# Optimization experiments

Measured on AMD Instinct MI355X. Metric: run time of the kernel, lower is better.

The kernel has to match this reference:

```python
import jax, jax.numpy as jnp
import numpy as np

N = 10000            # nodes
E = 320000           # edges (avg degree 32)
L = 4                # layers
S = 64               # hidden 0e multiplicity
V = 16               # hidden 1o multiplicity
EMB = 32             # node-attr embedding dim
NB = 8               # bessel basis per channel (r and v -> 2*NB edge feats)
MR = 2.5             # max_radius
DEG = 32.0           # num_neighbors
GS = S + V           # gate input scalars: 64 scalars + 16 gates
NW = S * 2 + V * 2 + V * 2   # 192 per-edge tensor-product weights
MAXT = 100           # max atom types


def _semi_unitary(K):
    # Newton-Schulz orthogonalization: K^T K -> I (semi-unitary uplift matrix)
    K = K / jnp.linalg.norm(K)
    for _ in range(10):
        K = 1.5 * K - 0.5 * K @ (K.T @ K)
    return K


def _smooth_cutoff(t):
    u = 2.0 * (t - 1.0)
    y = (1.0 - jnp.cos(jnp.pi * u)) * 0.5
    return jnp.where(u > 0, 0.0, jnp.where(u < -1.0, 1.0, y))


def _edge_geom(d):
    # d: (E,3) edge vector. Returns cutoff-weighted 1x1o SH (component norm) and bessel features.
    r = jnp.linalg.norm(d, axis=1)                       # (E,)
    sh = np.sqrt(3.0) * d / r[:, None]                   # spherical harmonics 1x1o
    attr = _smooth_cutoff(r / MR)[:, None] * sh          # (E,3)
    k = jnp.arange(1, NB + 1, dtype=jnp.float32) * jnp.pi
    feat = np.sqrt(2.0 / MR) * jnp.sin(k * (r / MR)[:, None]) / r[:, None]
    return attr, feat * np.sqrt(NB)                      # (E,3), (E,NB)


def _fctp(s, v, attr, Ws, Wv):
    # FullyConnectedTensorProduct with pure-scalar (0e) node attr == attr-weighted per-irrep linear
    os = jnp.einsum('ni,ne,oie->no', s, attr, Ws) / np.sqrt(s.shape[1] * EMB)
    ov = jnp.einsum('nim,ne,oie->nom', v, attr, Wv) / np.sqrt(v.shape[1] * EMB)
    return os, ov


def _forward(x, node_attr, edge_src, edge_dst, emb_table, PU_K, h, mix,
             si_Ws, si_Wv, sc_Ws, sc_Wv, lin1_Ws, lin1_Wv, lin2_Ws, lin2_Wv,
             fc_W1, fc_b1, fc_W2, fc_b2, fc_W3, fc_b3):
    attr = emb_table[node_attr]                          # (N,EMB)
    K = _semi_unitary(PU_K)                              # (V,2)
    yv = jnp.einsum('ui,nim->num', K, x.reshape(N, 2, 3))  # uplift vectors
    ys = jnp.zeros((N, S), x.dtype)
    ys_old, yv_old = ys, yv
    c_s, c_x = np.sin(np.pi / 8), np.cos(np.pi / 8)
    for i in range(L):
        ar, fr = _edge_geom(x[:, :3][edge_src] - x[:, :3][edge_dst])
        av, fv = _edge_geom(x[:, 3:][edge_src] - x[:, 3:][edge_dst])
        a = jnp.stack([ar, av], axis=1)                  # (E,2,3) = 2x1o edge attr
        ef = jnp.concatenate([fr, fv], axis=1)           # (E,2*NB)
        # radial MLP -> per-edge TP weights
        hd = jax.nn.silu(ef @ fc_W1[i] + fc_b1[i])
        hd = jax.nn.silu(hd @ fc_W2[i] + fc_b2[i])
        w = hd @ fc_W3[i] + fc_b3[i]                     # (E,NW)
        w1 = w[:, :S * 2].reshape(-1, S, 2)
        w2 = w[:, S * 2:S * 2 + V * 2].reshape(-1, V, 2)
        w3 = w[:, S * 2 + V * 2:].reshape(-1, V, 2)
        # conv: lin1 -> gather -> TP -> scatter -> lin2 ; plus self-connection
        fs, fvv = _fctp(ys, yv, attr, lin1_Ws[i], lin1_Wv[i])
        s_src, v_src = fs[edge_src], fvv[edge_src]
        # 0e x 1o -> 1o (uvu)
        o1 = jnp.einsum('euv,eu,evm->eum', w1, s_src, a) / np.sqrt(2.0)   # (E,S,3)
        # 1o x 1o -> 0e (uvu)
        dots = jnp.einsum('eum,evm->euv', v_src, a)
        o2 = jnp.einsum('euv,euv->eu', w2, dots) / np.sqrt(6.0)           # (E,V)
        # 1o x 1o -> 1o (cross, uvu)
        cr = jnp.cross(v_src[:, :, None, :], a[:, None, :, :])            # (E,V,2,3)
        o3 = jnp.einsum('euv,euvm->eum', w3, cr) / 2.0                    # (E,V,3)
        mid_s = jax.ops.segment_sum(o2, edge_dst, num_segments=N) / np.sqrt(DEG)
        mid_v = jax.ops.segment_sum(jnp.concatenate([o1, o3], axis=1), edge_dst,
                                    num_segments=N) / np.sqrt(DEG)        # (N,S+V,3)
        cs2, cv2 = _fctp(mid_s, mid_v, attr, lin2_Ws[i], lin2_Wv[i])      # (N,GS),(N,V,3)
        scs, scv = _fctp(ys, yv, attr, sc_Ws[i], sc_Wv[i])
        conv_s = c_s * scs + c_x * cs2
        conv_v = c_s * scv + c_x * cv2
        # gate: silu scalars, sigmoid gates * gated vectors
        gns = jax.nn.silu(conv_s[:, :S])
        gnv = jax.nn.sigmoid(conv_s[:, S:])[:, :, None] * conv_v
        # self-interaction: per-irrep linear
        sis = ys @ si_Ws[i].T / np.sqrt(S)
        siv = jnp.einsum('oi,nim->nom', si_Wv[i], yv) / np.sqrt(V)
        # leapfrog update
        h2 = h[i] ** 2
        ns = 2.0 * ys - ys_old + h2 * (mix[i] * gns + (mix[i] - 1.0) * sis)
        nv = 2.0 * yv - yv_old + h2 * (mix[i] * gnv + (mix[i] - 1.0) * siv)
        ys_old, yv_old = ys, yv
        ys, yv = ns, nv
        x = jnp.einsum('ui,num->nim', K, yv).reshape(N, 6)   # project
    return x


def setup_inputs() -> dict:
    key = jax.random.key(0)
    ks = jax.random.split(key, 24)
    def g(i, sh, fan=1.0):
        return jax.random.normal(ks[i], sh, dtype=jnp.float32) / np.sqrt(fan)
    edge_src = jax.random.randint(ks[20], (E,), 0, N, dtype=jnp.int32)
    off = jax.random.randint(ks[21], (E,), 1, N, dtype=jnp.int32)
    edge_dst = (edge_src + off) % N                      # guarantees src != dst
    return {
        'x': g(0, (N, 6)),
        'batch': jnp.zeros((N,), jnp.int32),
        'node_attr': jax.random.randint(ks[22], (N,), 0, MAXT, dtype=jnp.int32),
        'edge_src': edge_src,
        'edge_dst': edge_dst,
        'emb_table': g(1, (MAXT, EMB)),
        'PU_K': g(2, (V, 2)),
        'h': jnp.full((L,), 0.01, jnp.float32),
        'mix': jnp.full((L,), 0.5, jnp.float32),
        'si_Ws': g(3, (L, S, S)), 'si_Wv': g(4, (L, V, V)),
        'sc_Ws': g(5, (L, GS, S, EMB)), 'sc_Wv': g(6, (L, V, V, EMB)),
        'lin1_Ws': g(7, (L, S, S, EMB)), 'lin1_Wv': g(8, (L, V, V, EMB)),
        'lin2_Ws': g(9, (L, GS, V, EMB)), 'lin2_Wv': g(10, (L, V, S + V, EMB)),
        'fc_W1': g(11, (L, 2 * NB, 64), 2 * NB), 'fc_b1': jnp.zeros((L, 64), jnp.float32),
        'fc_W2': g(12, (L, 64, 64), 64), 'fc_b2': jnp.zeros((L, 64), jnp.float32),
        'fc_W3': g(13, (L, 64, NW), 64), 'fc_b3': jnp.zeros((L, NW), jnp.float32),
    }


def reference(x, batch, node_attr, edge_src, edge_dst, emb_table, PU_K, h, mix,
              si_Ws, si_Wv, sc_Ws, sc_Wv, lin1_Ws, lin1_Wv, lin2_Ws, lin2_Wv,
              fc_W1, fc_b1, fc_W2, fc_b2, fc_W3, fc_b3):
    return _forward(x, node_attr, edge_src, edge_dst, emb_table, PU_K, h, mix,
                    si_Ws, si_Wv, sc_Ws, sc_Wv, lin1_Ws, lin1_Wv, lin2_Ws, lin2_Wv,
                    fc_W1, fc_b1, fc_W2, fc_b2, fc_W3, fc_b3)
```

## Files before the change

### kernel.cpp

```cpp
#include <hip/hip_runtime.h>
#include <hip/hip_fp8.h>
#include <math.h>

#define NN 10000
#define NE 320000
#define PI_F 3.14159265358979323846f

typedef __attribute__((ext_vector_type(8))) short short8x;
typedef __attribute__((ext_vector_type(4))) float float4x;
typedef __attribute__((ext_vector_type(4))) unsigned short ushort4x;

#if defined(__has_builtin)
#if __has_builtin(__builtin_amdgcn_cvt_pk_fp8_f32) && __has_builtin(__builtin_amdgcn_cvt_f32_fp8)
#define HW_FP8 1
#endif
#endif

__device__ __forceinline__ unsigned short f2b(float f) {
    unsigned b = __float_as_uint(f);
    return (unsigned short)((b + 0x7FFFu + ((b >> 16) & 1u)) >> 16);
}
__device__ __forceinline__ float b2f(unsigned short u) {
    return __uint_as_float(((unsigned)u) << 16);
}
__device__ __forceinline__ float silu(float x) {
    return x / (1.f + __expf(-x));
}
__device__ __forceinline__ unsigned char f2e4(float f) {
#ifdef HW_FP8
    int r = __builtin_amdgcn_cvt_pk_fp8_f32(f, f, 0, false);
    return (unsigned char)(r & 0xff);
#else
    __hip_fp8_e4m3 q(f);
    return (unsigned char)q.__x;
#endif
}
__device__ __forceinline__ float e42f(unsigned char v) {
#ifdef HW_FP8
    return __builtin_amdgcn_cvt_f32_fp8((int)v, 0);
#else
    __hip_fp8_e4m3 q;
    q.__x = (__hip_fp8_storage_t)v;
    return (float)q;
#endif
}
__device__ __forceinline__ float e4sel(unsigned word, int sel) {
#ifdef HW_FP8
    switch (sel & 3) {
        case 0:  return __builtin_amdgcn_cvt_f32_fp8((int)word, 0);
        case 1:  return __builtin_amdgcn_cvt_f32_fp8((int)word, 1);
        case 2:  return __builtin_amdgcn_cvt_f32_fp8((int)word, 2);
        default: return __builtin_amdgcn_cvt_f32_fp8((int)word, 3);
    }
#else
    return e42f((unsigned char)((word >> (8*(sel & 3))) & 0xffu));
#endif
}
__device__ __forceinline__ unsigned pk4(float a, float b, float c, float d) {
#ifdef HW_FP8
    unsigned w = (unsigned)__builtin_amdgcn_cvt_pk_fp8_f32(a, b, 0, false);
    w = (unsigned)__builtin_amdgcn_cvt_pk_fp8_f32(c, d, (int)w, true);
    return w;
#else
    return (unsigned)f2e4(a) | ((unsigned)f2e4(b) << 8) |
           ((unsigned)f2e4(c) << 16) | ((unsigned)f2e4(d) << 24);
#endif
}

__global__ void k_newton_kernel(const float* __restrict__ PU, float* __restrict__ Kout)
{
    if (threadIdx.x != 0 || blockIdx.x != 0) return;
    float K[32];
    float nrm = 0.f;
    for (int i = 0; i < 32; ++i) { K[i] = PU[i]; nrm += K[i]*K[i]; }
    float inv = 1.0f / sqrtf(nrm);
    for (int i = 0; i < 32; ++i) K[i] *= inv;
    for (int it = 0; it < 10; ++it) {
        float m00 = 0.f, m01 = 0.f, m11 = 0.f;
        for (int u = 0; u < 16; ++u) {
            float a = K[2*u], b = K[2*u+1];
            m00 += a*a; m01 += a*b; m11 += b*b;
        }
        for (int u = 0; u < 16; ++u) {
            float a = K[2*u], b = K[2*u+1];
            K[2*u]   = 1.5f*a - 0.5f*(a*m00 + b*m01);
            K[2*u+1] = 1.5f*b - 0.5f*(a*m01 + b*m11);
        }
    }
    for (int i = 0; i < 32; ++i) Kout[i] = K[i];
}

__global__ __launch_bounds__(256) void init_all_kernel(
    const float* __restrict__ x, const float* __restrict__ K,
    float* __restrict__ xp, float* __restrict__ yv0, float* __restrict__ yv1,
    float* __restrict__ ys0, float* __restrict__ ys1, float* __restrict__ fsb)
{
    int tid = blockIdx.x*256 + threadIdx.x;
    if (tid < NN*8) {
        int n = tid >> 3, c = tid & 7;
        xp[tid] = (c < 6) ? x[n*6 + c] : 0.f;
        return;
    }
    int t2 = tid - NN*8;
    if (t2 < NN*48) {
        int n = t2/48, j = t2%48, u = j/3, m = j%3;
        float v = K[2*u]*x[n*6+m] + K[2*u+1]*x[n*6+3+m];
        yv0[t2] = v; yv1[t2] = v;
        return;
    }
    t2 -= NN*48;
    if (t2 < NN*64) { ys0[t2] = 0.f; ys1[t2] = 0.f; fsb[t2] = 0.f; }
}

__global__ void init_fvv_kernel(const float* __restrict__ yv, const int* __restrict__ types,
                                const float* __restrict__ lin1vT0, float* __restrict__ fvv)
{
    int tid = blockIdx.x*blockDim.x + threadIdx.x;
    if (tid >= NN*48) return;
    int n = tid/48, j = tid%48, o = j/3, m = j%3;
    int t = types[n];
    const float* W = lin1vT0 + (size_t)t*256;
    float acc = 0.f;
    #pragma unroll
    for (int i = 0; i < 16; ++i) acc += yv[n*48 + i*3 + m]*W[i*16 + o];
    fvv[tid] = acc;
}

__device__ __forceinline__ void be_body(const float* __restrict__ W, const float* __restrict__ emb,
                                        float* __restrict__ out, int id, int O, int I, float scale)
{
    int o = id % O; int r = id / O;
    int i = r % I; r /= I;
    int t = r % 100; int l = r / 100;
    const float* w  = W + (((size_t)l*O + o)*I + i)*32;
    const float* em = emb + (size_t)t*32;
    float acc = 0.f;
    #pragma unroll
    for (int e = 0; e < 32; ++e) acc += w[e]*em[e];
    out[id] = acc*scale;
}

#define PREP_TOTAL (2048000 + 1638400 + 512000 + 512000 + 102400 + 102400 + 49152 + 16384 + 16384 + 8192 + 1024)
__global__ __launch_bounds__(256) void prep_kernel(
    const float* __restrict__ lin1_Ws, const float* __restrict__ lin1_Wv,
    const float* __restrict__ sc_Ws,   const float* __restrict__ sc_Wv,
    const float* __restrict__ lin2_Ws, const float* __restrict__ lin2_Wv,
    const float* __restrict__ si_Ws,   const float* __restrict__ si_Wv,
    const float* __restrict__ fc_W1,   const float* __restrict__ fc_W2,
    const float* __restrict__ fc_W3,   const float* __restrict__ emb,
    float* __restrict__ lin1sT, float* __restrict__ lin1vT,
    float* __restrict__ scsT,   float* __restrict__ scvT,
    float* __restrict__ lin2sT, float* __restrict__ lin2vT,
    float* __restrict__ siWsT,  float* __restrict__ siWvT,
    unsigned short* __restrict__ w1bp, unsigned short* __restrict__ w2bp,
    unsigned short* __restrict__ w3bf)
{
    const float s2048 = 0.022097086912079608f;
    const float s512  = 0.044194173824159216f;
    const float s2560 = 0.019764235376052372f;
    int tid = blockIdx.x*256 + threadIdx.x;
    if (tid < 2048000) { be_body(sc_Ws,   emb, scsT,   tid, 80, 64, s2048); return; }
    tid -= 2048000;
    if (tid < 1638400) { be_body(lin1_Ws, emb, lin1sT, tid, 64, 64, s2048); return; }
    tid -= 1638400;
    if (tid < 512000)  { be_body(lin2_Ws, emb, lin2sT, tid, 80, 16, s512);  return; }
    tid -= 512000;
    if (tid < 512000)  { be_body(lin2_Wv, emb, lin2vT, tid, 16, 80, s2560); return; }
    tid -= 512000;
    if (tid < 102400)  { be_body(lin1_Wv, emb, lin1vT, tid, 16, 16, s512);  return; }
    tid -= 102400;
    if (tid < 102400)  { be_body(sc_Wv,   emb, scvT,   tid, 16, 16, s512);  return; }
    tid -= 102400;
    if (tid < 49152) {
        int o = tid % 64; int r = tid / 64; int i = r % 192; int l = r / 192;
        w3bf[tid] = f2b(fc_W3[((size_t)l*64 + o)*192 + i]);
        return;
    }
    tid -= 49152;
    if (tid < 16384) {
        int o = tid % 64; int r = tid / 64; int i = r % 64; int l = r / 64;
        siWsT[tid] = si_Ws[((size_t)l*64 + o)*64 + i]*0.125f;
        return;
    }
    tid -= 16384;
    if (tid < 16384) {
        int kk = tid % 64; int r = tid / 64; int n = r % 64; int l = r / 64;
        w2bp[tid] = f2b(fc_W2[((size_t)l*64 + kk)*64 + n]);
        return;
    }
    tid -= 16384;
    if (tid < 8192) {
        int kk = tid % 32; int r = tid / 32; int n = r % 64; int l = r / 64;
        float v = (kk < 16) ? fc_W1[((size_t)l*16 + kk)*64 + n] : 0.f;
        w1bp[tid] = f2b(v);
        return;
    }
    tid -= 8192;
    if (tid < 1024) {
        int o = tid % 16; int r = tid / 16; int i = r % 16; int l = r / 16;
        siWvT[tid] = si_Wv[((size_t)l*16 + o)*16 + i]*0.25f;
    }
}

__global__ void hist_kernel(const int* __restrict__ dst, int* __restrict__ deg)
{
    int e = blockIdx.x*256 + threadIdx.x;
    if (e < NE) atomicAdd(&deg[dst[e]], 1);
}

__global__ __launch_bounds__(256) void scan_kernel(const int* __restrict__ deg,
                                                   int* __restrict__ segoff,
                                                   int* __restrict__ cursor)
{
    __shared__ int part[256];
    int tid = threadIdx.x;
    int base = tid*40;
    int s = 0;
    for (int i = 0; i < 40; ++i) { int idx = base+i; if (idx < NN) s += deg[idx]; }
    part[tid] = s;
    __syncthreads();
    for (int o = 1; o < 256; o <<= 1) {
        int v = (tid >= o) ? part[tid-o] : 0;
        __syncthreads();
        part[tid] += v;
        __syncthreads();
    }
    int excl = part[tid] - s;
    for (int i = 0; i < 40; ++i) {
        int idx = base+i;
        if (idx < NN) { segoff[idx] = excl; cursor[idx] = excl; excl += deg[idx]; }
        else if (idx == NN) { segoff[NN] = excl; }
    }
}

__global__ void scatter_kernel(const int* __restrict__ src, const int* __restrict__ dst,
                               int* __restrict__ cursor,
                               int* __restrict__ srcs, int* __restrict__ dsts)
{
    int e = blockIdx.x*256 + threadIdx.x;
    if (e >= NE) return;
    int d = dst[e];
    int p = atomicAdd(&cursor[d], 1);
    srcs[p] = src[e]; dsts[p] = d;
}

__global__ __launch_bounds__(256, 5) void edge_fused_kernel(
    const float* __restrict__ xp,
    const int* __restrict__ srcs, const int* __restrict__ dsts,
    const unsigned short* __restrict__ w1b,
    const float* __restrict__ b1,
    const unsigned short* __restrict__ w2b,
    const float* __restrict__ b2,
    const unsigned short* __restrict__ w3b,
    const float* __restrict__ b3,
    const float* __restrict__ fs, const float* __restrict__ fvv,
    float* __restrict__ mid)
{
    __shared__ __align__(16) unsigned char smem[192*68];
    __shared__ unsigned short fsl[64][68];
    __shared__ unsigned short fvl[48][68];
    __shared__ float abuf[6][68];
    __shared__ int sdst[64];
    __shared__ unsigned smaskl[2];
    unsigned short* hbuf = (unsigned short*)smem;
    const float C3f = 0.08838834764831845f;
    int lane = threadIdx.x & 63;
    int wid  = threadIdx.x >> 6;
    int eblk = blockIdx.x * 64;
    int row16 = lane & 15, quad = lane >> 4;
    int erow = 16*wid + row16;

    if (threadIdx.x < 64) {
        int tid = threadIdx.x;
        int own = dsts[eblk + tid];
        int pidx = eblk + tid - ((tid > 0) ? 1 : 0);
        int prev = dsts[pidx];
        sdst[tid] = own;
        bool nb = (tid > 0) && (own != prev);
        unsigned long long bm = __ballot(nb);
        if (tid == 0) { smaskl[0] = (unsigned)bm; smaskl[1] = (unsigned)(bm >> 32); }
    }

    if (lane < 32) {
        int eidx = 16*wid + (lane & 15);
        int half = lane >> 4;
        int p = eblk + eidx;
        int s = srcs[p], d = dsts[p];
        int off = 3*half;
        const float* xs = xp + (size_t)s*8 + off;
        const float* xd = xp + (size_t)d*8 + off;
        float d0 = xs[0]-xd[0], d1 = xs[1]-xd[1], d2 = xs[2]-xd[2];
        float r = sqrtf(d0*d0 + d1*d1 + d2*d2);
        float invr = 1.0f/r;
        float u = 0.8f*r - 2.0f;
        float cut = (u > 0.f) ? 0.f : ((u < -1.f) ? 1.f : 0.5f*(1.f - __cosf(PI_F*u)));
        float sc = 1.7320508075688772f*cut*invr;
        abuf[off+0][eidx] = sc*d0;
        abuf[off+1][eidx] = sc*d1;
        abuf[off+2][eidx] = sc*d2;
        float fsc = 2.5298221281347035f*invr;
        float wr = 1.2566370614359172f*r;
        unsigned epk[4];
        #pragma unroll
        for (int k = 0; k < 4; ++k) {
            float e0 = fsc*__sinf((float)(2*k+1)*wr);
            float e1 = fsc*__sinf((float)(2*k+2)*wr);
            epk[k] = (unsigned)f2b(e0) | ((unsigned)f2b(e1) << 16);
        }
        uint4* hr = (uint4*)(hbuf + eidx*72);
        uint4 q; q.x = epk[0]; q.y = epk[1]; q.z = epk[2]; q.w = epk[3];
        hr[half] = q;
        uint4 qz; qz.x = 0; qz.y = 0; qz.z = 0; qz.w = 0;
        hr[2+half] = qz;
    } else {
        int eidx = 16*wid + (lane & 15);
        int half = (lane >> 4) & 1;
        int s = srcs[eblk + eidx];
        const float4* fp = (const float4*)(fs + (size_t)s*64 + half*32);
        #pragma unroll
        for (int g = 0; g < 8; ++g) {
            float4 t = fp[g];
            int u0 = half*32 + g*4;
            fsl[u0+0][eidx] = f2b(t.x*0.125f);
            fsl[u0+1][eidx] = f2b(t.y*0.125f);
            fsl[u0+2][eidx] = f2b(t.z*0.125f);
            fsl[u0+3][eidx] = f2b(t.w*0.125f);
        }
        const float4* vp = (const float4*)(fvv + (size_t)s*48 + half*24);
        #pragma unroll
        for (int g = 0; g < 6; ++g) {
            float4 t = vp[g];
            int j0 = half*24 + g*4;
            fvl[j0+0][eidx] = f2b(t.x*C3f);
            fvl[j0+1][eidx] = f2b(t.y*C3f);
            fvl[j0+2][eidx] = f2b(t.z*C3f);
            fvl[j0+3][eidx] = f2b(t.w*C3f);
        }
    }

    {
        short8x a = *(const short8x*)(hbuf + erow*72 + quad*8);
        float4x c[4];
        #pragma unroll
        for (int nt = 0; nt < 4; ++nt) {
            short8x b = *(const short8x*)(w1b + ((size_t)(nt*16 + row16))*32 + quad*8);
            c[nt] = __builtin_amdgcn_mfma_f32_16x16x32_bf16(a, b, (float4x){0.f,0.f,0.f,0.f}, 0, 0, 0);
        }
        #pragma unroll
        for (int nt = 0; nt < 4; ++nt) {
            float bias = b1[nt*16 + row16];
            #pragma unroll
            for (int r = 0; r < 4; ++r) {
                float h = silu(c[nt][r] + bias);
                hbuf[(16*wid + quad*4 + r)*72 + nt*16 + row16] = f2b(h);
            }
        }
    }
    {
        short8x a0v = *(const short8x*)(hbuf + erow*72 + 0*32 + quad*8);
        short8x a1v = *(const short8x*)(hbuf + erow*72 + 1*32 + quad*8);
        float4x c[4];
        #pragma unroll
        for (int nt = 0; nt < 4; ++nt) {
            short8x b0 = *(const short8x*)(w2b + ((size_t)(nt*16 + row16))*64 + 0*32 + quad*8);
            float4x t = __builtin_amdgcn_mfma_f32_16x16x32_bf16(a0v, b0, (float4x){0.f,0.f,0.f,0.f}, 0, 0, 0);
            short8x b1v = *(const short8x*)(w2b + ((size_t)(nt*16 + row16))*64 + 1*32 + quad*8);
            c[nt] = __builtin_amdgcn_mfma_f32_16x16x32_bf16(a1v, b1v, t, 0, 0, 0);
        }
        #pragma unroll
        for (int nt = 0; nt < 4; ++nt) {
            float bias = b2[nt*16 + row16];
            #pragma unroll
            for (int r = 0; r < 4; ++r) {
                float h = silu(c[nt][r] + bias);
                hbuf[(16*wid + quad*4 + r)*72 + nt*16 + row16] = f2b(h);
            }
        }
    }
    {
        short8x a0v = *(const short8x*)(hbuf + erow*72 + 0*32 + quad*8);
        short8x a1v = *(const short8x*)(hbuf + erow*72 + 1*32 + quad*8);
        __syncthreads();
        float4x acc[12];
        #pragma unroll
        for (int nt = 0; nt < 12; ++nt) {
            short8x b0 = *(const short8x*)(w3b + ((size_t)(nt*16 + row16))*64 + 0*32 + quad*8);
            float4x t = __builtin_amdgcn_mfma_f32_16x16x32_bf16(a0v, b0, (float4x){0.f,0.f,0.f,0.f}, 0, 0, 0);
            short8x b1v = *(const short8x*)(w3b + ((size_t)(nt*16 + row16))*64 + 1*32 + quad*8);
            acc[nt] = __builtin_amdgcn_mfma_f32_16x16x32_bf16(a1v, b1v, t, 0, 0, 0);
        }
        #pragma unroll
        for (int nt = 0; nt < 12; ++nt) {
            unsigned pw = pk4(acc[nt][0], acc[nt][1], acc[nt][2], acc[nt][3]);
            *(unsigned*)(smem + (size_t)(nt*16 + row16)*68 + 16*wid + quad*4) = pw;
        }
    }
    __syncthreads();

    {
        int qt = wid;
        int ebase = 16*qt;
        unsigned mk0 = __builtin_amdgcn_readfirstlane(smaskl[0]);
        unsigned mk1 = __builtin_amdgcn_readfirstlane(smaskl[1]);
        unsigned mkq = (((qt & 2) ? mk1 : mk0) >> (16*(qt & 1))) & 0xffffu;
        mkq &= ~1u;

        const unsigned char* w1p = smem + (size_t)(2*lane)*68;
        const unsigned short* f1p = &fsl[lane][0];
        float b1A = b3[2*lane], b1B = b3[2*lane+1];

        bool iso2 = lane < 16;
        int j3 = lane - 16;
        int u3 = j3 / 3;
        int m3 = j3 - 3*u3;
        int m1 = (m3 == 2) ? 0 : (m3 + 1);
        int m2 = 3 - m3 - m1;
        const unsigned char* wbp;
        const unsigned short* vAp;
        const unsigned short* vBp;
        const unsigned short* vCp;
        const float* aM1a; const float* aM2a; const float* aM1b; const float* aM2b;
        float bbA, bbB;
        if (iso2) {
            wbp = smem + (size_t)(128 + 2*lane)*68;
            vAp = &fvl[3*lane+0][0]; vBp = &fvl[3*lane+1][0]; vCp = &fvl[3*lane+2][0];
            aM1a = aM2a = aM1b = aM2b = &abuf[0][0];
            bbA = b3[128 + 2*lane]; bbB = b3[129 + 2*lane];
        } else {
            wbp = smem + (size_t)(160 + 2*u3)*68;
            vAp = &fvl[3*u3+m1][0]; vBp = &fvl[3*u3+m2][0]; vCp = &fvl[0][0];
            aM1a = &abuf[m1][0]; aM2a = &abuf[m2][0];
            aM1b = &abuf[3+m1][0]; aM2b = &abuf[3+m2][0];
            bbA = b3[160 + 2*u3]; bbB = b3[161 + 2*u3];
        }
        float FSb = iso2 ? 0.8164965809277259f : 1.0f;
        int cb = 192 + lane;

        float acc0 = 0.f, acc1 = 0.f, acc2 = 0.f, accb = 0.f;
        int dcur = sdst[ebase];

        #pragma unroll
        for (int ch = 0; ch < 4; ++ch) {
            int e4 = ebase + 4*ch;
            float4x a00 = *(const float4x*)(&abuf[0][e4]);
            float4x a01 = *(const float4x*)(&abuf[1][e4]);
            float4x a02 = *(const float4x*)(&abuf[2][e4]);
            float4x a10 = *(const float4x*)(&abuf[3][e4]);
            float4x a11 = *(const float4x*)(&abuf[4][e4]);
            float4x a12 = *(const float4x*)(&abuf[5][e4]);
            unsigned wa4 = *(const unsigned*)(w1p + e4);
            unsigned wb4 = *(const unsigned*)(w1p + 68 + e4);
            ushort4x f4 = *(const ushort4x*)(f1p + e4);
            float q10[4], q11[4], q12[4];
            #pragma unroll
            for (int k = 0; k < 4; ++k) {
                float f = b2f(f4[k]);
                float wa = (e4sel(wa4, k) + b1A)*f;
                float wb = (e4sel(wb4, k) + b1B)*f;
                q10[k] = wa*a00[k] + wb*a10[k];
                q11[k] = wa*a01[k] + wb*a11[k];
                q12[k] = wa*a02[k] + wb*a12[k];
            }
            float qb[4];
            unsigned wba4 = *(const unsigned*)(wbp + e4);
            unsigned wbb4 = *(const unsigned*)(wbp + 68 + e4);
            if (iso2) {
                ushort4x v04 = *(const ushort4x*)(vAp + e4);
                ushort4x v14 = *(const ushort4x*)(vBp + e4);
                ushort4x v24 = *(const ushort4x*)(vCp + e4);
                #pragma unroll
                for (int k = 0; k < 4; ++k) {
                    float v0 = b2f(v04[k]), v1 = b2f(v14[k]), v2 = b2f(v24[k]);
                    float dd0 = v0*a00[k] + v1*a01[k] + v2*a02[k];
                    float dd1 = v0*a10[k] + v1*a11[k] + v2*a12[k];
                    qb[k] = (e4sel(wba4,k)+bbA)*dd0 + (e4sel(wbb4,k)+bbB)*dd1;
                }
            } else {
                ushort4x va4 = *(const ushort4x*)(vAp + e4);
                ushort4x vb4 = *(const ushort4x*)(vBp + e4);
                float4x c1m1 = *(const float4x*)(aM1a + e4);
                float4x c1m2 = *(const float4x*)(aM2a + e4);
                float4x c2m1 = *(const float4x*)(aM1b + e4);
                float4x c2m2 = *(const float4x*)(aM2b + e4);
                #pragma unroll
                for (int k = 0; k < 4; ++k) {
                    float va = b2f(va4[k]), vb = b2f(vb4[k]);
                    float cx0 = va*c1m2[k] - vb*c1m1[k];
                    float cx1 = va*c2m2[k] - vb*c2m1[k];
                    qb[k] = (e4sel(wba4,k)+bbA)*cx0 + (e4sel(wbb4,k)+bbB)*cx1;
                }
            }
            unsigned mch = (mkq >> (4*ch)) & 15u;
            if (mch == 0) {
                acc0 += (q10[0] + q10[1]) + (q10[2] + q10[3]);
                acc1 += (q11[0] + q11[1]) + (q11[2] + q11[3]);
                acc2 += (q12[0] + q12[1]) + (q12[2] + q12[3]);
                accb += (qb[0] + qb[1]) + (qb[2] + qb[3]);
            } else {
                #pragma unroll
                for (int k = 0; k < 4; ++k) {
                    if (mch & (1u << k)) {
                        float* mrow = mid + (size_t)dcur*256;
                        atomicAdd(mrow + 3*lane + 0, acc0);
                        atomicAdd(mrow + 3*lane + 1, acc1);
                        atomicAdd(mrow + 3*lane + 2, acc2);
                        atomicAdd(mrow + cb, accb*FSb);
                        acc0 = acc1 = acc2 = accb = 0.f;
                        dcur = sdst[e4 + k];
                    }
                    acc0 += q10[k]; acc1 += q11[k]; acc2 += q12[k]; accb += qb[k];
                }
            }
        }
        {
            float* mrow = mid + (size_t)dcur*256;
            atomicAdd(mrow + 3*lane + 0, acc0);
            atomicAdd(mrow + 3*lane + 1, acc1);
            atomicAdd(mrow + 3*lane + 2, acc2);
            atomicAdd(mrow + cb, accb*FSb);
        }
    }
}

__global__ __launch_bounds__(256) void node_update_kernel(
    const float* __restrict__ ys, const float* __restrict__ yv,
    float* __restrict__ ys_old, float* __restrict__ yv_old,
    const float* __restrict__ mid,
    const int* __restrict__ types,
    const float* __restrict__ scsT, const float* __restrict__ scvT,
    const float* __restrict__ lin2sT, const float* __restrict__ lin2vT,
    const float* __restrict__ siWsT, const float* __restrict__ siWvT,
    const float* __restrict__ lin1sTn, const float* __restrict__ lin1vTn,
    const float* __restrict__ Kbuf,
    const float* __restrict__ hv, const float* __restrict__ mixv, int layer,
    float* __restrict__ fs_out, float* __restrict__ fvv_out,
    float* __restrict__ xpad, float* __restrict__ dout)
{
    int n = blockIdx.x;
    int lane = threadIdx.x;
    __shared__ float ys_l[64], yv_l[48], mids[16], midv[240];
    __shared__ float conv_s[80], conv_v[48], sis_l[64], siv_l[48], ysn[64], yvn[48];
    int t = types[n];
    {
        float v = mid[(size_t)n*256 + lane];
        if (lane < 192) midv[lane] = v;
        else if (lane < 208) mids[lane-192] = v;
        else midv[192 + (lane-208)] = v;
    }
    if (lane < 64) ys_l[lane] = ys[n*64 + lane];
    else if (lane < 112) yv_l[lane-64] = yv[n*48 + (lane-64)];
    __syncthreads();
    if (lane < 80) {
        const float* Wsc = scsT + (size_t)t*5120;
        const float* W2s = lin2sT + (size_t)t*1280;
        float a_sc = 0.f, a_2 = 0.f;
        #pragma unroll
        for (int i = 0; i < 64; ++i) a_sc += ys_l[i]*Wsc[i*80 + lane];
        #pragma unroll
        for (int i = 0; i < 16; ++i) a_2 += mids[i]*W2s[i*80 + lane];
        conv_s[lane] = 0.3826834323650898f*a_sc + 0.9238795325112867f*a_2;
    } else if (lane < 144) {
        int o = lane - 80;
        float a_si = 0.f;
        #pragma unroll
        for (int i = 0; i < 64; ++i) a_si += ys_l[i]*siWsT[i*64 + o];
        sis_l[o] = a_si;
    } else if (lane < 192) {
        int j = lane - 144, o = j/3, m = j%3;
        const float* Wsc = scvT + (size_t)t*256;
        const float* W2v = lin2vT + (size_t)t*1280;
        float a_sc = 0.f, a_2 = 0.f, a_si = 0.f;
        #pragma unroll
        for (int i = 0; i < 16; ++i) {
            float y = yv_l[i*3+m];
            a_sc += y*Wsc[i*16+o];
            a_si += y*siWvT[i*16+o];
        }
        #pragma unroll
        for (int i = 0; i < 80; ++i) a_2 += midv[i*3+m]*W2v[i*16+o];
        conv_v[j] = 0.3826834323650898f*a_sc + 0.9238795325112867f*a_2;
        siv_l[j] = a_si;
    }
    __syncthreads();
    float hh = hv[layer]; float h2c = hh*hh; float mx = mixv[layer];
    if (lane < 64) {
        float cs = conv_s[lane];
        float gns = cs/(1.f + __expf(-cs));
        float ns = 2.f*ys_l[lane] - ys_old[n*64+lane] + h2c*(mx*gns + (mx-1.f)*sis_l[lane]);
        ys_old[n*64+lane] = ns;
        ysn[lane] = ns;
    } else if (lane < 112) {
        int j = lane-64, o = j/3;
        float g = 1.f/(1.f + __expf(-conv_s[64+o]));
        float gnv = g*conv_v[j];
        float nv = 2.f*yv_l[j] - yv_old[n*48+j] + h2c*(mx*gnv + (mx-1.f)*siv_l[j]);
        yv_old[n*48+j] = nv;
        yvn[j] = nv;
    }
    __syncthreads();
    if (lane < 6) {
        int i = lane/3, m = lane%3;
        float acc = 0.f;
        #pragma unroll
        for (int u = 0; u < 16; ++u) acc += Kbuf[2*u+i]*yvn[u*3+m];
        xpad[n*8 + lane] = acc;
        if (dout) dout[n*6 + lane] = acc;
    }
    if (lane < 64) {
        const float* W = lin1sTn + (size_t)t*4096;
        float acc = 0.f;
        #pragma unroll
        for (int i = 0; i < 64; ++i) acc += ysn[i]*W[i*64 + lane];
        fs_out[n*64 + lane] = acc;
    } else if (lane < 112) {
        int j = lane - 64, o = j/3, m = j%3;
        const float* W = lin1vTn + (size_t)t*256;
        float acc = 0.f;
        #pragma unroll
        for (int i = 0; i < 16; ++i) acc += yvn[i*3+m]*W[i*16 + o];
        fvv_out[n*48 + j] = acc;
    }
}

extern "C" void kernel_launch(void* const* d_in, const int* in_sizes, int n_in,
                              void* d_out, int out_size, void* d_ws, size_t ws_size,
                              hipStream_t stream)
{
    const float* x_in   = (const float*)d_in[0];
    const int*   types  = (const int*)  d_in[2];
    const int*   esrc   = (const int*)  d_in[3];
    const int*   edst   = (const int*)  d_in[4];
    const float* emb    = (const float*)d_in[5];
    const float* PU     = (const float*)d_in[6];
    const float* hv     = (const float*)d_in[7];
    const float* mixv   = (const float*)d_in[8];
    const float* si_Ws  = (const float*)d_in[9];
    const float* si_Wv  = (const float*)d_in[10];
    const float* sc_Ws  = (const float*)d_in[11];
    const float* sc_Wv  = (const float*)d_in[12];
    const float* lin1_Ws= (const float*)d_in[13];
    const float* lin1_Wv= (const float*)d_in[14];
    const float* lin2_Ws= (const float*)d_in[15];
    const float* lin2_Wv= (const float*)d_in[16];
    const float* fc_W1  = (const float*)d_in[17];
    const float* fc_b1  = (const float*)d_in[18];
    const float* fc_W2  = (const float*)d_in[19];
    const float* fc_b2  = (const float*)d_in[20];
    const float* fc_W3  = (const float*)d_in[21];
    const float* fc_b3  = (const float*)d_in[22];

    float* ws = (float*)d_ws;
    size_t off = 0;
    auto alloc = [&](size_t nf) { float* p = ws + off; off += nf; return p; };
    float* Kbuf   = alloc(64);
    float* x_pad  = alloc(80000);
    float* ys0    = alloc(640000);
    float* ys1    = alloc(640000);
    float* yv0    = alloc(480000);
    float* yv1    = alloc(480000);
    float* fsb    = alloc(640000);
    float* fvvb   = alloc(480000);
    float* midb   = alloc((size_t)NN*256);
    float* lin1sT = alloc((size_t)4*100*4096);
    float* lin1vT = alloc((size_t)4*100*256);
    float* scsT   = alloc((size_t)4*100*5120);
    float* scvT   = alloc((size_t)4*100*256);
    float* lin2sT = alloc((size_t)4*100*1280);
    float* lin2vT = alloc((size_t)4*100*1280);
    float* siWsT  = alloc((size_t)4*4096);
    float* siWvT  = alloc((size_t)4*256);
    int* iws = (int*)(ws + off);
    size_t ioff = 0;
    auto ialloc = [&](size_t ni) { int* p = iws + ioff; ioff += ni; return p; };
    int* deg    = ialloc(NN);
    int* segoff = ialloc(NN + 8);
    int* cursor = ialloc(NN);
    int* srcs   = ialloc(NE);
    int* dsts   = ialloc(NE);
    unsigned short* w1bp = (unsigned short*)(iws + ioff);
    unsigned short* w2bp = w1bp + (size_t)4*64*32;
    unsigned short* w3bf = w2bp + (size_t)4*64*64;

    k_newton_kernel<<<1, 1, 0, stream>>>(PU, Kbuf);
    prep_kernel<<<(PREP_TOTAL + 255)/256, 256, 0, stream>>>(
        lin1_Ws, lin1_Wv, sc_Ws, sc_Wv, lin2_Ws, lin2_Wv, si_Ws, si_Wv,
        fc_W1, fc_W2, fc_W3, emb,
        lin1sT, lin1vT, scsT, scvT, lin2sT, lin2vT, siWsT, siWvT,
        w1bp, w2bp, w3bf);
    {
        int tot = NN*8 + NN*48 + NN*64;
        init_all_kernel<<<(tot + 255)/256, 256, 0, stream>>>(
            x_in, Kbuf, x_pad, yv0, yv1, ys0, ys1, fsb);
    }
    init_fvv_kernel<<<(NN*48 + 255)/256, 256, 0, stream>>>(yv0, types, lin1vT, fvvb);

    (void)hipMemsetAsync(deg, 0, NN*sizeof(int), stream);
    hist_kernel<<<(NE+255)/256, 256, 0, stream>>>(edst, deg);
    scan_kernel<<<1, 256, 0, stream>>>(deg, segoff, cursor);
    scatter_kernel<<<(NE+255)/256, 256, 0, stream>>>(esrc, edst, cursor, srcs, dsts);

    float* ys_cur = ys0; float* ys_old = ys1;
    float* yv_cur = yv0; float* yv_old = yv1;
    for (int l = 0; l < 4; ++l) {
        (void)hipMemsetAsync(midb, 0, (size_t)NN*256*sizeof(float), stream);
        edge_fused_kernel<<<NE/64, 256, 0, stream>>>(
            x_pad, srcs, dsts,
            w1bp + (size_t)l*64*32,  fc_b1 + (size_t)l*64,
            w2bp + (size_t)l*64*64,  fc_b2 + (size_t)l*64,
            w3bf + (size_t)l*192*64, fc_b3 + (size_t)l*192,
            fsb, fvvb, midb);
        int ln = (l + 1) & 3;
        node_update_kernel<<<NN, 256, 0, stream>>>(
            ys_cur, yv_cur, ys_old, yv_old,
            midb, types,
            scsT   + (size_t)l*100*5120, scvT   + (size_t)l*100*256,
            lin2sT + (size_t)l*100*1280, lin2vT + (size_t)l*100*1280,
            siWsT  + (size_t)l*4096,     siWvT  + (size_t)l*256,
            lin1sT + (size_t)ln*100*4096, lin1vT + (size_t)ln*100*256,
            Kbuf, hv, mixv, l, fsb, fvvb,
            x_pad, (l == 3) ? (float*)d_out : nullptr);
        float* tmp;
        tmp = ys_cur; ys_cur = ys_old; ys_old = tmp;
        tmp = yv_cur; yv_cur = yv_old; yv_old = tmp;
    }
}
```

Baseline: 1.031 ms.

## Split edge scatter phase across waves by output irrep instead of edge quarter

Before, each of four waves handled 16 edges and computed both the l=1 vector outputs and the second-path outputs, with divergent branches inside a wave. Now waves 0-1 handle only the first path over 32 edges each, and waves 2-3 handle only the second path. The second path also merges the dot-product and cross-product variants into one branchless formula using sign and gamma factors. This is meant to cut per-wave register pressure and in-wave divergence, at the cost of uneven work between the two wave groups and extra zero-multiplied loads in the cross-product lanes.

```diff
diff --git a/kernel.cpp b/kernel.cpp
--- a/kernel.cpp
+++ b/kernel.cpp
@@ -398,126 +398,136 @@
     __syncthreads();
 
     {
-        int qt = wid;
-        int ebase = 16*qt;
         unsigned mk0 = __builtin_amdgcn_readfirstlane(smaskl[0]);
         unsigned mk1 = __builtin_amdgcn_readfirstlane(smaskl[1]);
-        unsigned mkq = (((qt & 2) ? mk1 : mk0) >> (16*(qt & 1))) & 0xffffu;
-        mkq &= ~1u;
-
-        const unsigned char* w1p = smem + (size_t)(2*lane)*68;
-        const unsigned short* f1p = &fsl[lane][0];
-        float b1A = b3[2*lane], b1B = b3[2*lane+1];
-
-        bool iso2 = lane < 16;
-        int j3 = lane - 16;
-        int u3 = j3 / 3;
-        int m3 = j3 - 3*u3;
-        int m1 = (m3 == 2) ? 0 : (m3 + 1);
-        int m2 = 3 - m3 - m1;
-        const unsigned char* wbp;
-        const unsigned short* vAp;
-        const unsigned short* vBp;
-        const unsigned short* vCp;
-        const float* aM1a; const float* aM2a; const float* aM1b; const float* aM2b;
-        float bbA, bbB;
-        if (iso2) {
-            wbp = smem + (size_t)(128 + 2*lane)*68;
-            vAp = &fvl[3*lane+0][0]; vBp = &fvl[3*lane+1][0]; vCp = &fvl[3*lane+2][0];
-            aM1a = aM2a = aM1b = aM2b = &abuf[0][0];
-            bbA = b3[128 + 2*lane]; bbB = b3[129 + 2*lane];
-        } else {
-            wbp = smem + (size_t)(160 + 2*u3)*68;
-            vAp = &fvl[3*u3+m1][0]; vBp = &fvl[3*u3+m2][0]; vCp = &fvl[0][0];
-            aM1a = &abuf[m1][0]; aM2a = &abuf[m2][0];
-            aM1b = &abuf[3+m1][0]; aM2b = &abuf[3+m2][0];
-            bbA = b3[160 + 2*u3]; bbB = b3[161 + 2*u3];
-        }
-        float FSb = iso2 ? 0.8164965809277259f : 1.0f;
-        int cb = 192 + lane;
-
-        float acc0 = 0.f, acc1 = 0.f, acc2 = 0.f, accb = 0.f;
+        bool iso1 = (wid < 2);
+        int h = iso1 ? wid : (wid - 2);
+        unsigned mkh = (h ? mk1 : mk0) & ~1u;
+        int ebase = 32*h;
         int dcur = sdst[ebase];
 
-        #pragma unroll
-        for (int ch = 0; ch < 4; ++ch) {
-            int e4 = ebase + 4*ch;
-            float4x a00 = *(const float4x*)(&abuf[0][e4]);
-            float4x a01 = *(const float4x*)(&abuf[1][e4]);
-            float4x a02 = *(const float4x*)(&abuf[2][e4]);
-            float4x a10 = *(const float4x*)(&abuf[3][e4]);
-            float4x a11 = *(const float4x*)(&abuf[4][e4]);
-            float4x a12 = *(const float4x*)(&abuf[5][e4]);
-            unsigned wa4 = *(const unsigned*)(w1p + e4);
-            unsigned wb4 = *(const unsigned*)(w1p + 68 + e4);
-            ushort4x f4 = *(const ushort4x*)(f1p + e4);
-            float q10[4], q11[4], q12[4];
+        if (iso1) {
+            const unsigned char* wp = smem + (size_t)(2*lane)*68;
+            const unsigned short* fp = &fsl[lane][0];
+            float bA = b3[2*lane], bB = b3[2*lane+1];
+            float acc0 = 0.f, acc1 = 0.f, acc2 = 0.f;
             #pragma unroll
-            for (int k = 0; k < 4; ++k) {
-                float f = b2f(f4[k]);
-                float wa = (e4sel(wa4, k) + b1A)*f;
-                float wb = (e4sel(wb4, k) + b1B)*f;
-                q10[k] = wa*a00[k] + wb*a10[k];
-                q11[k] = wa*a01[k] + wb*a11[k];
-                q12[k] = wa*a02[k] + wb*a12[k];
-            }
-            float qb[4];
-            unsigned wba4 = *(const unsigned*)(wbp + e4);
-            unsigned wbb4 = *(const unsigned*)(wbp + 68 + e4);
-            if (iso2) {
-                ushort4x v04 = *(const ushort4x*)(vAp + e4);
-                ushort4x v14 = *(const ushort4x*)(vBp + e4);
-                ushort4x v24 = *(const ushort4x*)(vCp + e4);
+            for (int ch = 0; ch < 8; ++ch) {
+                int e4 = ebase + 4*ch;
+                unsigned wa4 = *(const unsigned*)(wp + e4);
+                unsigned wb4 = *(const unsigned*)(wp + 68 + e4);
+                ushort4x f4 = *(const ushort4x*)(fp + e4);
+                float4x a00 = *(const float4x*)(&abuf[0][e4]);
+                float4x a01 = *(const float4x*)(&abuf[1][e4]);
+                float4x a02 = *(const float4x*)(&abuf[2][e4]);
+                float4x a10 = *(const float4x*)(&abuf[3][e4]);
+                float4x a11 = *(const float4x*)(&abuf[4][e4]);
+                float4x a12 = *(const float4x*)(&abuf[5][e4]);
+                float q0[4], q1[4], q2[4];
                 #pragma unroll
                 for (int k = 0; k < 4; ++k) {
-                    float v0 = b2f(v04[k]), v1 = b2f(v14[k]), v2 = b2f(v24[k]);
-                    float dd0 = v0*a00[k] + v1*a01[k] + v2*a02[k];
-                    float dd1 = v0*a10[k] + v1*a11[k] + v2*a12[k];
-                    qb[k] = (e4sel(wba4,k)+bbA)*dd0 + (e4sel(wbb4,k)+bbB)*dd1;
+                    float f = b2f(f4[k]);
+                    float wa = (e4sel(wa4, k) + bA)*f;
+                    float wb = (e4sel(wb4, k) + bB)*f;
+                    q0[k] = wa*a00[k] + wb*a10[k];
+                    q1[k] = wa*a01[k] + wb*a11[k];
+                    q2[k] = wa*a02[k] + wb*a12[k];
                 }
-            } else {
-                ushort4x va4 = *(const ushort4x*)(vAp + e4);
-                ushort4x vb4 = *(const ushort4x*)(vBp + e4);
-                float4x c1m1 = *(const float4x*)(aM1a + e4);
-                float4x c1m2 = *(const float4x*)(aM2a + e4);
-                float4x c2m1 = *(const float4x*)(aM1b + e4);
-                float4x c2m2 = *(const float4x*)(aM2b + e4);
-                #pragma unroll
-                for (int k = 0; k < 4; ++k) {
-                    float va = b2f(va4[k]), vb = b2f(vb4[k]);
-                    float cx0 = va*c1m2[k] - vb*c1m1[k];
-                    float cx1 = va*c2m2[k] - vb*c2m1[k];
-                    qb[k] = (e4sel(wba4,k)+bbA)*cx0 + (e4sel(wbb4,k)+bbB)*cx1;
+                unsigned mch = (mkh >> (4*ch)) & 15u;
+                if (mch == 0) {
+                    acc0 += (q0[0] + q0[1]) + (q0[2] + q0[3]);
+                    acc1 += (q1[0] + q1[1]) + (q1[2] + q1[3]);
+                    acc2 += (q2[0] + q2[1]) + (q2[2] + q2[3]);
+                } else {
+                    #pragma unroll
+                    for (int k = 0; k < 4; ++k) {
+                        if (mch & (1u << k)) {
+                            float* mrow = mid + (size_t)dcur*256;
+                            atomicAdd(mrow + 3*lane + 0, acc0);
+                            atomicAdd(mrow + 3*lane + 1, acc1);
+                            atomicAdd(mrow + 3*lane + 2, acc2);
+                            acc0 = acc1 = acc2 = 0.f;
+                            dcur = sdst[e4 + k];
+                        }
+                        acc0 += q0[k]; acc1 += q1[k]; acc2 += q2[k];
+                    }
                 }
             }
-            unsigned mch = (mkq >> (4*ch)) & 15u;
-            if (mch == 0) {
-                acc0 += (q10[0] + q10[1]) + (q10[2] + q10[3]);
-                acc1 += (q11[0] + q11[1]) + (q11[2] + q11[3]);
-                acc2 += (q12[0] + q12[1]) + (q12[2] + q12[3]);
-                accb += (qb[0] + qb[1]) + (qb[2] + qb[3]);
-            } else {
-                #pragma unroll
-                for (int k = 0; k < 4; ++k) {
-                    if (mch & (1u << k)) {
-                        float* mrow = mid + (size_t)dcur*256;
-                        atomicAdd(mrow + 3*lane + 0, acc0);
-                        atomicAdd(mrow + 3*lane + 1, acc1);
-                        atomicAdd(mrow + 3*lane + 2, acc2);
-                        atomicAdd(mrow + cb, accb*FSb);
-                        acc0 = acc1 = acc2 = accb = 0.f;
-                        dcur = sdst[e4 + k];
-                    }
-                    acc0 += q10[k]; acc1 += q11[k]; acc2 += q12[k]; accb += qb[k];
-                }
-            }
-        }
-        {
             float* mrow = mid + (size_t)dcur*256;
             atomicAdd(mrow + 3*lane + 0, acc0);
             atomicAdd(mrow + 3*lane + 1, acc1);
             atomicAdd(mrow + 3*lane + 2, acc2);
-            atomicAdd(mrow + cb, accb*FSb);
+        } else {
+            bool iso2 = lane < 16;
+            int j3 = lane - 16;
+            int u3 = j3 / 3;
+            int m3 = j3 - 3*u3;
+            int m1 = (m3 == 2) ? 0 : (m3 + 1);
+            int m2 = 3 - m3 - m1;
+            const unsigned char* wp;
+            const unsigned short* vAp; const unsigned short* vBp; const unsigned short* vCp;
+            const float* aX0; const float* aY0; const float* aZ0;
+            const float* aX1; const float* aY1; const float* aZ1;
+            float bA, bB, sgn, gam, FS;
+            if (iso2) {
+                wp = smem + (size_t)(128 + 2*lane)*68;
+                bA = b3[128 + 2*lane]; bB = b3[129 + 2*lane];
+                vAp = &fvl[3*lane+0][0]; vBp = &fvl[3*lane+1][0]; vCp = &fvl[3*lane+2][0];
+                aX0 = &abuf[0][0]; aY0 = &abuf[1][0]; aZ0 = &abuf[2][0];
+                aX1 = &abuf[3][0]; aY1 = &abuf[4][0]; aZ1 = &abuf[5][0];
+                sgn = 1.f; gam = 1.f; FS = 0.8164965809277259f;
+            } else {
+                wp = smem + (size_t)(160 + 2*u3)*68;
+                bA = b3[160 + 2*u3]; bB = b3[161 + 2*u3];
+                vAp = &fvl[3*u3+m1][0]; vBp = &fvl[3*u3+m2][0]; vCp = &fvl[0][0];
+                aX0 = &abuf[m2][0]; aY0 = &abuf[m1][0]; aZ0 = &abuf[0][0];
+                aX1 = &abuf[3+m2][0]; aY1 = &abuf[3+m1][0]; aZ1 = &abuf[3][0];
+                sgn = -1.f; gam = 0.f; FS = 1.f;
+            }
+            int cb = 192 + lane;
+            float accb = 0.f;
+            #pragma unroll
+            for (int ch = 0; ch < 8; ++ch) {
+                int e4 = ebase + 4*ch;
+                unsigned wa4 = *(const unsigned*)(wp + e4);
+                unsigned wb4 = *(const unsigned*)(wp + 68 + e4);
+                ushort4x vA4 = *(const ushort4x*)(vAp + e4);
+                ushort4x vB4 = *(const ushort4x*)(vBp + e4);
+                ushort4x vC4 = *(const ushort4x*)(vCp + e4);
+                float4x x0 = *(const float4x*)(aX0 + e4);
+                float4x y0 = *(const float4x*)(aY0 + e4);
+                float4x z0 = *(const float4x*)(aZ0 + e4);
+                float4x x1 = *(const float4x*)(aX1 + e4);
+                float4x y1 = *(const float4x*)(aY1 + e4);
+                float4x z1 = *(const float4x*)(aZ1 + e4);
+                float q[4];
+                #pragma unroll
+                for (int k = 0; k < 4; ++k) {
+                    float fa = b2f(vA4[k]);
+                    float fb = b2f(vB4[k]);
+                    float fc = b2f(vC4[k]);
+                    float dA = fmaf(sgn, fb*y0[k], fa*x0[k]);
+                    dA = fmaf(gam, fc*z0[k], dA);
+                    float dB = fmaf(sgn, fb*y1[k], fa*x1[k]);
+                    dB = fmaf(gam, fc*z1[k], dB);
+                    q[k] = (e4sel(wa4, k) + bA)*dA + (e4sel(wb4, k) + bB)*dB;
+                }
+                unsigned mch = (mkh >> (4*ch)) & 15u;
+                if (mch == 0) {
+                    accb += (q[0] + q[1]) + (q[2] + q[3]);
+                } else {
+                    #pragma unroll
+                    for (int k = 0; k < 4; ++k) {
+                        if (mch & (1u << k)) {
+                            atomicAdd(mid + (size_t)dcur*256 + cb, accb*FS);
+                            accb = 0.f;
+                            dcur = sdst[e4 + k];
+                        }
+                        accb += q[k];
+                    }
+                }
+            }
+            atomicAdd(mid + (size_t)dcur*256 + cb, accb*FS);
         }
     }
 }
```

After: 940.2 us. 1.1x faster.
